# Kernel tuning notes

Hardware: AMD Instinct MI355X
Metric: run time of the kernel (lower is better)

The kernel has to match this reference:

```python
import jax, jax.numpy as jnp
import numpy as np

B, T, C, H = 8, 1024, 1024, 16
NEG = -1000000000.0
EPS = 1e-12


def setup_inputs() -> dict:
    key = jax.random.key(0)
    ks = jax.random.split(key, 12)
    s = 0.02  # keep pre-softmax logits in a sane range
    return {
        "x": jax.random.normal(ks[0], (B, T, C), jnp.float32),
        "mask": jax.random.randint(ks[1], (B, T), 0, 2, jnp.int32),
        "Wq": jax.random.normal(ks[2], (C, C), jnp.float32) * s,
        "bq": jax.random.normal(ks[3], (C,), jnp.float32) * s,
        "Wk": jax.random.normal(ks[4], (C, C), jnp.float32) * s,
        "bk": jax.random.normal(ks[5], (C,), jnp.float32) * s,
        "Wv": jax.random.normal(ks[6], (C, C), jnp.float32) * s,
        "bv": jax.random.normal(ks[7], (C,), jnp.float32) * s,
        "Wp": jax.random.normal(ks[8], (C, C), jnp.float32) * s,
        "bp": jax.random.normal(ks[9], (C,), jnp.float32) * s,
        "ln_w": jnp.ones((C,), jnp.float32),
        "ln_b": jnp.zeros((C,), jnp.float32),
    }


def reference(x, mask, Wq, bq, Wk, bk, Wv, bv, Wp, bp, ln_w, ln_b):
    Bx, Tx, Cx = x.shape
    hd = Cx // H
    # torch nn.Linear: y = x @ W.T + b
    def lin(inp, W, b):
        return inp @ W.T + b

    def split_heads(t):  # [B,T,C] -> [B,H,T,hd]
        return t.reshape(Bx, Tx, H, hd).transpose(0, 2, 1, 3)

    q = split_heads(lin(x, Wq, bq))
    k = split_heads(lin(x, Wk, bk))
    v = split_heads(lin(x, Wv, bv))

    att = jnp.einsum("bhqd,bhkd->bhqk", q, k) * (1.0 / jnp.sqrt(jnp.float32(hd)))
    # mask [B,T] masks key positions; broadcast to [B,1,1,T]
    att = jnp.where(mask[:, None, None, :] == 0, NEG, att)
    # stable softmax (manual max-subtract, matching original)
    att = jax.nn.softmax(att, axis=-1)
    # dropout prob 0.0 -> identity (eval-mode faithful)
    y = jnp.einsum("bhqk,bhkd->bhqd", att, v)
    y = y.transpose(0, 2, 1, 3).reshape(Bx, Tx, Cx)
    y = lin(y, Wp, bp)
    # residual + LayerNorm(eps=1e-12)
    z = y + x
    mu = jnp.mean(z, axis=-1, keepdims=True)
    var = jnp.mean(jnp.square(z - mu), axis=-1, keepdims=True)
    out = (z - mu) * jax.lax.rsqrt(var + EPS) * ln_w + ln_b
    return out
```

## Files before the change

kernel.cpp:

```cpp
#include <hip/hip_runtime.h>
#include <stdint.h>

#define B_ 8
#define T_ 1024
#define C_ 1024
#define H_ 16
#define HD 64
#define M_TOT (B_ * T_)

using f32x4 = __attribute__((ext_vector_type(4))) float;
using s16x8 = __attribute__((ext_vector_type(8))) short;
using i32x4 = __attribute__((ext_vector_type(4))) int;

__device__ __forceinline__ unsigned short f2bf(float f) {
  unsigned int u = __builtin_bit_cast(unsigned int, f);
  unsigned int r = (u + 0x7fffu + ((u >> 16) & 1u)) >> 16;
  return (unsigned short)r;
}
__device__ __forceinline__ float bf2f(unsigned short s) {
  unsigned int u = ((unsigned int)s) << 16;
  return __builtin_bit_cast(float, u);
}

__device__ __forceinline__ void gload_lds16(const void* g, void* l) {
  __builtin_amdgcn_global_load_lds(
      (const __attribute__((address_space(1))) unsigned int*)g,
      (__attribute__((address_space(3))) unsigned int*)l, 16, 0, 0);
}

__global__ __launch_bounds__(256) void k_convert(
    const float* __restrict__ x, const float* __restrict__ wq,
    const float* __restrict__ wk, const float* __restrict__ wv,
    const float* __restrict__ wp, const float* __restrict__ bq,
    const float* __restrict__ bk, const float* __restrict__ bv,
    const int* __restrict__ maskp, unsigned short* __restrict__ xb,
    unsigned short* __restrict__ wqkv, unsigned short* __restrict__ wpb,
    float* __restrict__ bias_cat, unsigned int* __restrict__ mpair) {
  const long n_x = (long)M_TOT * C_;
  const long W_ELT = (long)C_ * C_;
  const long total4 = (n_x + 4 * W_ELT) >> 2;
  for (long i4 = (long)blockIdx.x * blockDim.x + threadIdx.x; i4 < total4;
       i4 += (long)gridDim.x * blockDim.x) {
    long i = i4 << 2;
    const float* src;
    unsigned short* dst;
    if (i < n_x) {
      src = x + i;
      dst = xb + i;
    } else {
      long off = i - n_x;
      int which = (int)(off >> 20);
      long wo = off & (W_ELT - 1);
      if (which < 3) {
        src = (which == 0 ? wq : which == 1 ? wk : wv) + wo;
        dst = wqkv + which * W_ELT + wo;
      } else {
        src = wp + wo;
        dst = wpb + wo;
      }
    }
    float4 v = *(const float4*)src;
    ushort4 u;
    u.x = f2bf(v.x); u.y = f2bf(v.y); u.z = f2bf(v.z); u.w = f2bf(v.w);
    *(ushort4*)dst = u;
  }
  int t = blockIdx.x * blockDim.x + threadIdx.x;
  if (t < 3 * C_) {
    float v = t < C_ ? bq[t] : (t < 2 * C_ ? bk[t - C_] : bv[t - 2 * C_]);
    bias_cat[t] = v;
  }
  if (t < B_ * T_ / 2) {
    const int* mr = maskp + t * 2;
    mpair[t] = (mr[0] ? 0xFFFFu : 0u) | (mr[1] ? 0xFFFF0000u : 0u);
  }
}

template <int EPI>
__global__ __launch_bounds__(256, 2) void k_gemm(
    const unsigned short* __restrict__ A, const unsigned short* __restrict__ Bm,
    const float* __restrict__ bias, unsigned short* __restrict__ q_ws,
    unsigned short* __restrict__ k_ws, unsigned short* __restrict__ vt_ws,
    const unsigned short* __restrict__ xres16, unsigned short* __restrict__ z16) {
  __shared__ unsigned short Al[2][128 * 64];
  __shared__ unsigned short Bl[2][128 * 64];
  const int tid = threadIdx.x, lane = tid & 63, w = tid >> 6;
  const int lc = lane & 15, lr = lane >> 4;
  const int wm = w >> 1, wn = w & 1;
  const int GX = (EPI == 0) ? 24 : 8;
  const int NWG = GX * 64;
  int flat = blockIdx.y * GX + blockIdx.x;
  int swz = (flat & 7) * (NWG / 8) + (flat >> 3);
  const int m0 = (swz / GX) * 128, n0 = (swz % GX) * 128;
  const char* Ab = (const char*)A;
  const char* Bb = (const char*)Bm;

  f32x4 acc[4][4] = {};

  auto stage = [&](int buf, int kt) {
#pragma unroll
    for (int i = 0; i < 4; ++i) {
      int g = i * 256 + tid;
      int row = g >> 3, gr = g & 7;
      gload_lds16(Ab + (long)(m0 + row) * 2048 + kt * 128 + ((gr ^ (row & 7)) << 4),
                  (char*)Al[buf] + (i * 256 + w * 64) * 16);
    }
#pragma unroll
    for (int i = 0; i < 4; ++i) {
      int g = i * 256 + tid;
      int row = g >> 3, gr = g & 7;
      gload_lds16(Bb + (long)(n0 + row) * 2048 + kt * 128 + ((gr ^ (row & 7)) << 4),
                  (char*)Bl[buf] + (i * 256 + w * 64) * 16);
    }
  };

  stage(0, 0);
  stage(1, 1);
  asm volatile("s_waitcnt vmcnt(8)" ::: "memory");
  __builtin_amdgcn_sched_barrier(0);
  __builtin_amdgcn_s_barrier();
  __builtin_amdgcn_sched_barrier(0);

#pragma unroll
  for (int kt = 0; kt < 16; ++kt) {
    const int cur = kt & 1;
    const char* Ac = (const char*)Al[cur];
    const char* Bc = (const char*)Bl[cur];
    s16x8 af0[4], bf0[4];
#pragma unroll
    for (int mf = 0; mf < 4; ++mf) {
      int ar = wm * 64 + mf * 16 + lc;
      af0[mf] = *(const s16x8*)(Ac + ar * 128 + ((lr ^ (ar & 7)) << 4));
    }
#pragma unroll
    for (int nf = 0; nf < 4; ++nf) {
      int br = wn * 64 + nf * 16 + lc;
      bf0[nf] = *(const s16x8*)(Bc + br * 128 + ((lr ^ (br & 7)) << 4));
    }
#pragma unroll
    for (int mf = 0; mf < 4; ++mf)
#pragma unroll
      for (int nf = 0; nf < 4; ++nf)
        acc[mf][nf] = __builtin_amdgcn_mfma_f32_16x16x32_bf16(af0[mf], bf0[nf],
                                                              acc[mf][nf], 0, 0, 0);
    s16x8 af1[4], bf1[4];
#pragma unroll
    for (int mf = 0; mf < 4; ++mf) {
      int ar = wm * 64 + mf * 16 + lc;
      af1[mf] = *(const s16x8*)(Ac + ar * 128 + (((4 + lr) ^ (ar & 7)) << 4));
    }
#pragma unroll
    for (int nf = 0; nf < 4; ++nf) {
      int br = wn * 64 + nf * 16 + lc;
      bf1[nf] = *(const s16x8*)(Bc + br * 128 + (((4 + lr) ^ (br & 7)) << 4));
    }
    asm volatile("s_waitcnt lgkmcnt(0)" ::: "memory");
    __builtin_amdgcn_sched_barrier(0);
    __builtin_amdgcn_s_barrier();
    __builtin_amdgcn_sched_barrier(0);
    if (kt + 2 < 16) stage(cur, kt + 2);
    __builtin_amdgcn_s_setprio(1);
#pragma unroll
    for (int mf = 0; mf < 4; ++mf)
#pragma unroll
      for (int nf = 0; nf < 4; ++nf)
        acc[mf][nf] = __builtin_amdgcn_mfma_f32_16x16x32_bf16(af1[mf], bf1[nf],
                                                              acc[mf][nf], 0, 0, 0);
    __builtin_amdgcn_s_setprio(0);
    if (kt + 2 < 16)
      asm volatile("s_waitcnt vmcnt(8)" ::: "memory");
    else
      asm volatile("s_waitcnt vmcnt(0)" ::: "memory");
    __builtin_amdgcn_sched_barrier(0);
    __builtin_amdgcn_s_barrier();
    __builtin_amdgcn_sched_barrier(0);
  }

  if (EPI == 0) {
#pragma unroll
    for (int mf = 0; mf < 4; ++mf)
#pragma unroll
      for (int nf = 0; nf < 4; ++nf) {
        int gn = n0 + wn * 64 + nf * 16 + lc;
        int which = gn >> 10, nn = gn & 1023;
        int hh = nn >> 6, dd = nn & 63;
        float bia = bias[gn];
        if (which == 2) {
          int gm = m0 + wm * 64 + mf * 16 + lr * 4;
          int bb = gm >> 10, tt = gm & 1023;
          ushort4 pk;
          pk.x = f2bf(acc[mf][nf][0] + bia);
          pk.y = f2bf(acc[mf][nf][1] + bia);
          pk.z = f2bf(acc[mf][nf][2] + bia);
          pk.w = f2bf(acc[mf][nf][3] + bia);
          *(ushort4*)&vt_ws[((long)(bb * H_ + hh) * HD + dd) * T_ + tt] = pk;
        } else {
          unsigned short* dst = (which == 0) ? q_ws : k_ws;
          float scl = (which == 0) ? 0.18033688011112042f : 1.0f;
#pragma unroll
          for (int i = 0; i < 4; ++i) {
            int gm = m0 + wm * 64 + mf * 16 + lr * 4 + i;
            int bb = gm >> 10, tt = gm & 1023;
            dst[((long)(bb * H_ + hh) * T_ + tt) * HD + dd] =
                f2bf((acc[mf][nf][i] + bia) * scl);
          }
        }
      }
  } else {
#pragma unroll
    for (int mf = 0; mf < 4; ++mf)
#pragma unroll
      for (int nf = 0; nf < 4; ++nf) {
        int gn = n0 + wn * 64 + nf * 16 + lc;
        float bia = bias[gn];
#pragma unroll
        for (int i = 0; i < 4; ++i) {
          int gm = m0 + wm * 64 + mf * 16 + lr * 4 + i;
          long idx = (long)gm * C_ + gn;
          z16[idx] = f2bf(acc[mf][nf][i] + bia + bf2f(xres16[idx]));
        }
      }
  }
}

__global__ __launch_bounds__(256, 2) void k_attn(
    const unsigned short* __restrict__ Qp, const unsigned short* __restrict__ Kp,
    const unsigned short* __restrict__ Vtp, const unsigned int* __restrict__ mpairp,
    unsigned short* __restrict__ Yp) {
  __shared__ unsigned short Kl[2][64 * 64];
  __shared__ unsigned short Vl[2][64 * 64];
  const int tid = threadIdx.x, lane = tid & 63, w = tid >> 6;
  const int bid = blockIdx.x;
  const int xcd = bid & 7, slot = bid >> 3;
  const int bh = xcd * 16 + (slot >> 2);
  const int qt = slot & 3;
  const int b = bh >> 4, h = bh & 15;
  const int lc = lane & 15, lr = lane >> 4;
  const int q0 = qt * 256 + w * 64;

  const unsigned short* qbase = Qp + ((long)bh * T_ + q0) * HD;
  s16x8 aq[4][2];
#pragma unroll
  for (int g = 0; g < 4; ++g) {
    aq[g][0] = *(const s16x8*)(qbase + (g * 16 + lc) * HD + lr * 8);
    aq[g][1] = *(const s16x8*)(qbase + (g * 16 + lc) * HD + 32 + lr * 8);
  }

  s16x8 ones;
#pragma unroll
  for (int j = 0; j < 8; ++j) ones[j] = (short)0x3F80;

  f32x4 o[4][4] = {};
  f32x4 ol[4] = {};

  const char* kb_g = (const char*)(Kp + (long)bh * T_ * HD);
  const char* vb_g = (const char*)(Vtp + (long)bh * HD * T_);
  const unsigned int* mrow2 = mpairp + b * (T_ / 2);

  auto stage = [&](int buf, int kt) {
#pragma unroll
    for (int it = 0; it < 2; ++it) {
      int f = it * 4096 + w * 1024 + lane * 16;
      int row = f >> 7;
      int swz = (f & 127) ^ ((row & 7) << 4);
      gload_lds16(kb_g + (long)kt * 8192 + (f & ~127) + swz,
                  (char*)Kl[buf] + it * 4096 + w * 1024);
      gload_lds16(vb_g + (long)row * (T_ * 2) + kt * 128 + swz,
                  (char*)Vl[buf] + it * 4096 + w * 1024);
    }
  };

  stage(0, 0);
  __syncthreads();

  const int s01 = lc + ((lane & 16) << 1);
  const int s23 = s01 + 16;
  const bool hi = (lane >= 32);

  int cur = 0;
  for (int kt = 0; kt < T_ / 64; ++kt) {
    if (kt + 1 < T_ / 64) stage(cur ^ 1, kt + 1);

    f32x4 s[4][4];
    const char* kl = (const char*)Kl[cur];
#pragma unroll
    for (int kf = 0; kf < 4; ++kf) {
      int key = kf * 16 + lc;
      s16x8 kb0 = *(const s16x8*)(kl + ((key * 128 + lr * 16) ^ ((key & 7) << 4)));
      s16x8 kb1 = *(const s16x8*)(kl + ((key * 128 + 64 + lr * 16) ^ ((key & 7) << 4)));
#pragma unroll
      for (int g = 0; g < 4; ++g) {
        f32x4 z = {};
        z = __builtin_amdgcn_mfma_f32_16x16x32_bf16(kb0, aq[g][0], z, 0, 0, 0);
        z = __builtin_amdgcn_mfma_f32_16x16x32_bf16(kb1, aq[g][1], z, 0, 0, 0);
        s[g][kf] = z;
      }
    }

    unsigned int mw[4][2];
#pragma unroll
    for (int kf = 0; kf < 4; ++kf) {
      mw[kf][0] = mrow2[kt * 32 + kf * 8 + lr * 2];
      mw[kf][1] = mrow2[kt * 32 + kf * 8 + lr * 2 + 1];
    }

    unsigned int pk[4][4][2];
#pragma unroll
    for (int g = 0; g < 4; ++g)
#pragma unroll
      for (int kf = 0; kf < 4; ++kf) {
        unsigned int u0 = __builtin_bit_cast(unsigned int, __builtin_amdgcn_exp2f(s[g][kf][0]));
        unsigned int u1 = __builtin_bit_cast(unsigned int, __builtin_amdgcn_exp2f(s[g][kf][1]));
        unsigned int u2 = __builtin_bit_cast(unsigned int, __builtin_amdgcn_exp2f(s[g][kf][2]));
        unsigned int u3 = __builtin_bit_cast(unsigned int, __builtin_amdgcn_exp2f(s[g][kf][3]));
        pk[g][kf][0] = ((u1 & 0xFFFF0000u) | (u0 >> 16)) & mw[kf][0];
        pk[g][kf][1] = ((u3 & 0xFFFF0000u) | (u2 >> 16)) & mw[kf][1];
      }

#pragma unroll
    for (int kc = 0; kc < 2; ++kc) {
      s16x8 ap[4];
#pragma unroll
      for (int g = 0; g < 4; ++g) {
        unsigned int A0 = pk[g][kc * 2][0], A1 = pk[g][kc * 2][1];
        unsigned int B0 = pk[g][kc * 2 + 1][0], B1 = pk[g][kc * 2 + 1][1];
        unsigned int w0a = __shfl((int)A0, s01, 64), w0b = __shfl((int)B0, s01, 64);
        unsigned int w1a = __shfl((int)A1, s01, 64), w1b = __shfl((int)B1, s01, 64);
        unsigned int w2a = __shfl((int)A0, s23, 64), w2b = __shfl((int)B0, s23, 64);
        unsigned int w3a = __shfl((int)A1, s23, 64), w3b = __shfl((int)B1, s23, 64);
        i32x4 wv;
        wv[0] = (int)(hi ? w0b : w0a);
        wv[1] = (int)(hi ? w1b : w1a);
        wv[2] = (int)(hi ? w2b : w2a);
        wv[3] = (int)(hi ? w3b : w3a);
        ap[g] = __builtin_bit_cast(s16x8, wv);
      }
      int koff = kc * 64 + lr * 16;
      __builtin_amdgcn_s_setprio(1);
#pragma unroll
      for (int g = 0; g < 4; ++g)
        ol[g] = __builtin_amdgcn_mfma_f32_16x16x32_bf16(ones, ap[g], ol[g], 0, 0, 0);
#pragma unroll
      for (int nf = 0; nf < 4; ++nf) {
        int drow = nf * 16 + lc;
        s16x8 vb = *(const s16x8*)((const char*)Vl[cur] +
                                   ((drow * 128 + koff) ^ ((drow & 7) << 4)));
#pragma unroll
        for (int g = 0; g < 4; ++g)
          o[g][nf] = __builtin_amdgcn_mfma_f32_16x16x32_bf16(vb, ap[g], o[g][nf], 0, 0, 0);
      }
      __builtin_amdgcn_s_setprio(0);
    }
    __syncthreads();
    cur ^= 1;
  }

#pragma unroll
  for (int g = 0; g < 4; ++g) {
    float rl = 1.0f / ol[g][0];
    unsigned short* yrow = Yp + ((long)(b * T_ + q0 + g * 16 + lc)) * C_ + h * 64;
#pragma unroll
    for (int nf = 0; nf < 4; ++nf) {
      ushort4 pw;
      pw.x = f2bf(o[g][nf][0] * rl);
      pw.y = f2bf(o[g][nf][1] * rl);
      pw.z = f2bf(o[g][nf][2] * rl);
      pw.w = f2bf(o[g][nf][3] * rl);
      *(ushort4*)(yrow + nf * 16 + lr * 4) = pw;
    }
  }
}

__global__ __launch_bounds__(256) void k_ln(const unsigned short* __restrict__ z16,
                                            const float* __restrict__ lw,
                                            const float* __restrict__ lb,
                                            float* __restrict__ out) {
  const int row = blockIdx.x;
  ushort4 v16 = ((const ushort4*)(z16 + (long)row * C_))[threadIdx.x];
  float4 v;
  v.x = bf2f(v16.x); v.y = bf2f(v16.y); v.z = bf2f(v16.z); v.w = bf2f(v16.w);
  float s = v.x + v.y + v.z + v.w;
  float s2 = v.x * v.x + v.y * v.y + v.z * v.z + v.w * v.w;
#pragma unroll
  for (int d = 1; d < 64; d <<= 1) {
    s += __shfl_xor(s, d, 64);
    s2 += __shfl_xor(s2, d, 64);
  }
  __shared__ float rs[4], rq[4];
  int wv_ = threadIdx.x >> 6;
  if ((threadIdx.x & 63) == 0) { rs[wv_] = s; rq[wv_] = s2; }
  __syncthreads();
  s = rs[0] + rs[1] + rs[2] + rs[3];
  s2 = rq[0] + rq[1] + rq[2] + rq[3];
  float mu = s * (1.0f / C_);
  float var = s2 * (1.0f / C_) - mu * mu;
  float inv = rsqrtf(var + 1e-12f);
  float4 wv4 = ((const float4*)lw)[threadIdx.x];
  float4 bv4 = ((const float4*)lb)[threadIdx.x];
  float4 ov;
  ov.x = (v.x - mu) * inv * wv4.x + bv4.x;
  ov.y = (v.y - mu) * inv * wv4.y + bv4.y;
  ov.z = (v.z - mu) * inv * wv4.z + bv4.z;
  ov.w = (v.w - mu) * inv * wv4.w + bv4.w;
  ((float4*)(out + (long)row * C_))[threadIdx.x] = ov;
}

extern "C" void kernel_launch(void* const* d_in, const int* in_sizes, int n_in,
                              void* d_out, int out_size, void* d_ws,
                              size_t ws_size, hipStream_t stream) {
  const float* x = (const float*)d_in[0];
  const int* mask = (const int*)d_in[1];
  const float* Wq = (const float*)d_in[2];
  const float* bq = (const float*)d_in[3];
  const float* Wk = (const float*)d_in[4];
  const float* bk = (const float*)d_in[5];
  const float* Wv = (const float*)d_in[6];
  const float* bv = (const float*)d_in[7];
  const float* Wp = (const float*)d_in[8];
  const float* bp = (const float*)d_in[9];
  const float* lnw = (const float*)d_in[10];
  const float* lnb = (const float*)d_in[11];
  float* out = (float*)d_out;

  char* ws = (char*)d_ws;
  const size_t MB = 1024 * 1024;
  unsigned short* xb = (unsigned short*)(ws);
  unsigned short* q_ws = (unsigned short*)(ws + 16 * MB);
  unsigned short* k_ws = (unsigned short*)(ws + 32 * MB);
  unsigned short* vt_ws = (unsigned short*)(ws + 48 * MB);
  unsigned short* y_ws = (unsigned short*)(ws + 64 * MB);
  unsigned short* wqkv = (unsigned short*)(ws + 80 * MB);
  unsigned short* wpb = (unsigned short*)(ws + 86 * MB);
  float* bias_cat = (float*)(ws + 88 * MB);
  unsigned int* mpair = (unsigned int*)(ws + 88 * MB + 16384);
  unsigned short* z16 = (unsigned short*)(ws + 48 * MB);

  k_convert<<<dim3(2048), dim3(256), 0, stream>>>(x, Wq, Wk, Wv, Wp, bq, bk, bv,
                                                  mask, xb, wqkv, wpb, bias_cat,
                                                  mpair);
  k_gemm<0><<<dim3(24, 64), dim3(256), 0, stream>>>(
      xb, wqkv, bias_cat, q_ws, k_ws, vt_ws, nullptr, nullptr);
  k_attn<<<dim3(512), dim3(256), 0, stream>>>(q_ws, k_ws, vt_ws, mpair, y_ws);
  k_gemm<1><<<dim3(8, 64), dim3(256), 0, stream>>>(
      y_ws, wpb, bp, nullptr, nullptr, nullptr, xb, z16);
  k_ln<<<dim3(8192), dim3(256), 0, stream>>>(z16, lnw, lnb, out);
}
```

Measured before the change: 163.9 us.

## Use 256x256 tiles with 8 waves and interleaved staging for QKV GEMM

Splits the QKV projection into its own kernel with 256x256 output tiles, 512 threads (8 waves in a 2x4 layout), and a 384-block grid. Global-to-LDS loads for the next k-step are split into four quarter stages and interleaved with four MFMA sub-phases, each wave holding 8x4 accumulators. The larger tile raises arithmetic intensity and reuse of the staged A and B tiles. In exchange it uses 128 KB of LDS per block, more registers, and fewer blocks, so wave-level parallelism and occupancy drop.

```diff
diff --git a/kernel.cpp b/kernel.cpp
--- a/kernel.cpp
+++ b/kernel.cpp
@@ -75,18 +75,193 @@
   }
 }
 
-template <int EPI>
-__global__ __launch_bounds__(256, 2) void k_gemm(
+__global__ __launch_bounds__(512, 2) void k_gemm_qkv(
     const unsigned short* __restrict__ A, const unsigned short* __restrict__ Bm,
     const float* __restrict__ bias, unsigned short* __restrict__ q_ws,
-    unsigned short* __restrict__ k_ws, unsigned short* __restrict__ vt_ws,
-    const unsigned short* __restrict__ xres16, unsigned short* __restrict__ z16) {
+    unsigned short* __restrict__ k_ws, unsigned short* __restrict__ vt_ws) {
+  __shared__ unsigned short Al[2][256 * 64];
+  __shared__ unsigned short Bl[2][256 * 64];
+  const int tid = threadIdx.x, lane = tid & 63, w = tid >> 6;
+  const int lc = lane & 15, lr = lane >> 4;
+  const int wm = w >> 2, wn = w & 3;
+  const int GX = 12;
+  const int NWG = GX * 32;
+  int flat = blockIdx.y * GX + blockIdx.x;
+  int swz = (flat & 7) * (NWG / 8) + (flat >> 3);
+  const int m0 = (swz / GX) * 256, n0 = (swz % GX) * 256;
+  const char* Ab = (const char*)A;
+  const char* Bb = (const char*)Bm;
+
+  f32x4 acc[8][4] = {};
+
+  auto stageA = [&](int buf, int kt, int half) {
+#pragma unroll
+    for (int j = 0; j < 2; ++j) {
+      int i = half * 2 + j;
+      int g = i * 512 + tid;
+      int row = g >> 3, gr = g & 7;
+      gload_lds16(Ab + (long)(m0 + row) * 2048 + kt * 128 + ((gr ^ (row & 7)) << 4),
+                  (char*)Al[buf] + (long)(i * 512 + w * 64) * 16);
+    }
+  };
+  auto stageB = [&](int buf, int kt, int half) {
+#pragma unroll
+    for (int j = 0; j < 2; ++j) {
+      int i = half * 2 + j;
+      int g = i * 512 + tid;
+      int row = g >> 3, gr = g & 7;
+      gload_lds16(Bb + (long)(n0 + row) * 2048 + kt * 128 + ((gr ^ (row & 7)) << 4),
+                  (char*)Bl[buf] + (long)(i * 512 + w * 64) * 16);
+    }
+  };
+
+  stageA(0, 0, 0);
+  stageB(0, 0, 0);
+  stageA(0, 0, 1);
+  stageB(0, 0, 1);
+
+#pragma unroll
+  for (int kt = 0; kt < 16; ++kt) {
+    const int cur = kt & 1, nxt = cur ^ 1;
+    const bool have = (kt + 1 < 16);
+    const char* Ac = (const char*)Al[cur];
+    const char* Bc = (const char*)Bl[cur];
+    s16x8 aLo[4][2], aHi[4][2], bfr[4][2];
+
+    if (have) stageA(nxt, kt + 1, 0);
+    if (have)
+      asm volatile("s_waitcnt vmcnt(2)" ::: "memory");
+    else
+      asm volatile("s_waitcnt vmcnt(0)" ::: "memory");
+    __builtin_amdgcn_sched_barrier(0);
+    __builtin_amdgcn_s_barrier();
+    __builtin_amdgcn_sched_barrier(0);
+#pragma unroll
+    for (int mf = 0; mf < 4; ++mf) {
+      int ar = wm * 128 + mf * 16 + lc;
+#pragma unroll
+      for (int kk = 0; kk < 2; ++kk)
+        aLo[mf][kk] = *(const s16x8*)(Ac + ar * 128 + (((kk * 4 + lr) ^ (ar & 7)) << 4));
+    }
+#pragma unroll
+    for (int nf = 0; nf < 2; ++nf) {
+      int br = wn * 64 + nf * 16 + lc;
+#pragma unroll
+      for (int kk = 0; kk < 2; ++kk)
+        bfr[nf][kk] = *(const s16x8*)(Bc + br * 128 + (((kk * 4 + lr) ^ (br & 7)) << 4));
+    }
+    asm volatile("s_waitcnt lgkmcnt(0)" ::: "memory");
+    __builtin_amdgcn_sched_barrier(0);
+    __builtin_amdgcn_s_setprio(1);
+#pragma unroll
+    for (int mf = 0; mf < 4; ++mf)
+#pragma unroll
+      for (int nf = 0; nf < 2; ++nf)
+#pragma unroll
+        for (int kk = 0; kk < 2; ++kk)
+          acc[mf][nf] = __builtin_amdgcn_mfma_f32_16x16x32_bf16(
+              aLo[mf][kk], bfr[nf][kk], acc[mf][nf], 0, 0, 0);
+    __builtin_amdgcn_s_setprio(0);
+
+    if (have) stageB(nxt, kt + 1, 0);
+#pragma unroll
+    for (int nf = 2; nf < 4; ++nf) {
+      int br = wn * 64 + nf * 16 + lc;
+#pragma unroll
+      for (int kk = 0; kk < 2; ++kk)
+        bfr[nf][kk] = *(const s16x8*)(Bc + br * 128 + (((kk * 4 + lr) ^ (br & 7)) << 4));
+    }
+    asm volatile("s_waitcnt lgkmcnt(0)" ::: "memory");
+    __builtin_amdgcn_sched_barrier(0);
+    __builtin_amdgcn_s_setprio(1);
+#pragma unroll
+    for (int mf = 0; mf < 4; ++mf)
+#pragma unroll
+      for (int nf = 2; nf < 4; ++nf)
+#pragma unroll
+        for (int kk = 0; kk < 2; ++kk)
+          acc[mf][nf] = __builtin_amdgcn_mfma_f32_16x16x32_bf16(
+              aLo[mf][kk], bfr[nf][kk], acc[mf][nf], 0, 0, 0);
+    __builtin_amdgcn_s_setprio(0);
+
+    if (have) stageA(nxt, kt + 1, 1);
+#pragma unroll
+    for (int mf = 0; mf < 4; ++mf) {
+      int ar = wm * 128 + 64 + mf * 16 + lc;
+#pragma unroll
+      for (int kk = 0; kk < 2; ++kk)
+        aHi[mf][kk] = *(const s16x8*)(Ac + ar * 128 + (((kk * 4 + lr) ^ (ar & 7)) << 4));
+    }
+    asm volatile("s_waitcnt lgkmcnt(0)" ::: "memory");
+    __builtin_amdgcn_sched_barrier(0);
+    __builtin_amdgcn_s_setprio(1);
+#pragma unroll
+    for (int mf = 0; mf < 4; ++mf)
+#pragma unroll
+      for (int nf = 2; nf < 4; ++nf)
+#pragma unroll
+        for (int kk = 0; kk < 2; ++kk)
+          acc[4 + mf][nf] = __builtin_amdgcn_mfma_f32_16x16x32_bf16(
+              aHi[mf][kk], bfr[nf][kk], acc[4 + mf][nf], 0, 0, 0);
+    __builtin_amdgcn_s_setprio(0);
+
+    if (have) stageB(nxt, kt + 1, 1);
+    __builtin_amdgcn_s_setprio(1);
+#pragma unroll
+    for (int mf = 0; mf < 4; ++mf)
+#pragma unroll
+      for (int nf = 0; nf < 2; ++nf)
+#pragma unroll
+        for (int kk = 0; kk < 2; ++kk)
+          acc[4 + mf][nf] = __builtin_amdgcn_mfma_f32_16x16x32_bf16(
+              aHi[mf][kk], bfr[nf][kk], acc[4 + mf][nf], 0, 0, 0);
+    __builtin_amdgcn_s_setprio(0);
+    __builtin_amdgcn_sched_barrier(0);
+    __builtin_amdgcn_s_barrier();
+    __builtin_amdgcn_sched_barrier(0);
+  }
+
+#pragma unroll
+  for (int mf = 0; mf < 8; ++mf)
+#pragma unroll
+    for (int nf = 0; nf < 4; ++nf) {
+      int gn = n0 + wn * 64 + nf * 16 + lc;
+      int which = gn >> 10, nn = gn & 1023;
+      int hh = nn >> 6, dd = nn & 63;
+      float bia = bias[gn];
+      if (which == 2) {
+        int gm = m0 + wm * 128 + mf * 16 + lr * 4;
+        int bb = gm >> 10, tt = gm & 1023;
+        ushort4 pk;
+        pk.x = f2bf(acc[mf][nf][0] + bia);
+        pk.y = f2bf(acc[mf][nf][1] + bia);
+        pk.z = f2bf(acc[mf][nf][2] + bia);
+        pk.w = f2bf(acc[mf][nf][3] + bia);
+        *(ushort4*)&vt_ws[((long)(bb * H_ + hh) * HD + dd) * T_ + tt] = pk;
+      } else {
+        unsigned short* dst = (which == 0) ? q_ws : k_ws;
+        float scl = (which == 0) ? 0.18033688011112042f : 1.0f;
+#pragma unroll
+        for (int i = 0; i < 4; ++i) {
+          int gm = m0 + wm * 128 + mf * 16 + lr * 4 + i;
+          int bb = gm >> 10, tt = gm & 1023;
+          dst[((long)(bb * H_ + hh) * T_ + tt) * HD + dd] =
+              f2bf((acc[mf][nf][i] + bia) * scl);
+        }
+      }
+    }
+}
+
+__global__ __launch_bounds__(256, 2) void k_gemm_proj(
+    const unsigned short* __restrict__ A, const unsigned short* __restrict__ Bm,
+    const float* __restrict__ bias, const unsigned short* __restrict__ xres16,
+    unsigned short* __restrict__ z16) {
   __shared__ unsigned short Al[2][128 * 64];
   __shared__ unsigned short Bl[2][128 * 64];
   const int tid = threadIdx.x, lane = tid & 63, w = tid >> 6;
   const int lc = lane & 15, lr = lane >> 4;
   const int wm = w >> 1, wn = w & 1;
-  const int GX = (EPI == 0) ? 24 : 8;
+  const int GX = 8;
   const int NWG = GX * 64;
   int flat = blockIdx.y * GX + blockIdx.x;
   int swz = (flat & 7) * (NWG / 8) + (flat >> 3);
@@ -175,51 +350,19 @@
     __builtin_amdgcn_sched_barrier(0);
   }
 
-  if (EPI == 0) {
-#pragma unroll
-    for (int mf = 0; mf < 4; ++mf)
-#pragma unroll
-      for (int nf = 0; nf < 4; ++nf) {
-        int gn = n0 + wn * 64 + nf * 16 + lc;
-        int which = gn >> 10, nn = gn & 1023;
-        int hh = nn >> 6, dd = nn & 63;
-        float bia = bias[gn];
-        if (which == 2) {
-          int gm = m0 + wm * 64 + mf * 16 + lr * 4;
-          int bb = gm >> 10, tt = gm & 1023;
-          ushort4 pk;
-          pk.x = f2bf(acc[mf][nf][0] + bia);
-          pk.y = f2bf(acc[mf][nf][1] + bia);
-          pk.z = f2bf(acc[mf][nf][2] + bia);
-          pk.w = f2bf(acc[mf][nf][3] + bia);
-          *(ushort4*)&vt_ws[((long)(bb * H_ + hh) * HD + dd) * T_ + tt] = pk;
-        } else {
-          unsigned short* dst = (which == 0) ? q_ws : k_ws;
-          float scl = (which == 0) ? 0.18033688011112042f : 1.0f;
-#pragma unroll
-          for (int i = 0; i < 4; ++i) {
-            int gm = m0 + wm * 64 + mf * 16 + lr * 4 + i;
-            int bb = gm >> 10, tt = gm & 1023;
-            dst[((long)(bb * H_ + hh) * T_ + tt) * HD + dd] =
-                f2bf((acc[mf][nf][i] + bia) * scl);
-          }
-        }
-      }
-  } else {
-#pragma unroll
-    for (int mf = 0; mf < 4; ++mf)
-#pragma unroll
-      for (int nf = 0; nf < 4; ++nf) {
-        int gn = n0 + wn * 64 + nf * 16 + lc;
-        float bia = bias[gn];
-#pragma unroll
-        for (int i = 0; i < 4; ++i) {
-          int gm = m0 + wm * 64 + mf * 16 + lr * 4 + i;
-          long idx = (long)gm * C_ + gn;
-          z16[idx] = f2bf(acc[mf][nf][i] + bia + bf2f(xres16[idx]));
-        }
-      }
-  }
+#pragma unroll
+  for (int mf = 0; mf < 4; ++mf)
+#pragma unroll
+    for (int nf = 0; nf < 4; ++nf) {
+      int gn = n0 + wn * 64 + nf * 16 + lc;
+      float bia = bias[gn];
+#pragma unroll
+      for (int i = 0; i < 4; ++i) {
+        int gm = m0 + wm * 64 + mf * 16 + lr * 4 + i;
+        long idx = (long)gm * C_ + gn;
+        z16[idx] = f2bf(acc[mf][nf][i] + bia + bf2f(xres16[idx]));
+      }
+    }
 }
 
 __global__ __launch_bounds__(256, 2) void k_attn(
@@ -437,10 +580,9 @@
   k_convert<<<dim3(2048), dim3(256), 0, stream>>>(x, Wq, Wk, Wv, Wp, bq, bk, bv,
                                                   mask, xb, wqkv, wpb, bias_cat,
                                                   mpair);
-  k_gemm<0><<<dim3(24, 64), dim3(256), 0, stream>>>(
-      xb, wqkv, bias_cat, q_ws, k_ws, vt_ws, nullptr, nullptr);
+  k_gemm_qkv<<<dim3(12, 32), dim3(512), 0, stream>>>(xb, wqkv, bias_cat, q_ws,
+                                                     k_ws, vt_ws);
   k_attn<<<dim3(512), dim3(256), 0, stream>>>(q_ws, k_ws, vt_ws, mpair, y_ws);
-  k_gemm<1><<<dim3(8, 64), dim3(256), 0, stream>>>(
-      y_ws, wpb, bp, nullptr, nullptr, nullptr, xb, z16);
+  k_gemm_proj<<<dim3(8, 64), dim3(256), 0, stream>>>(y_ws, wpb, bp, xb, z16);
   k_ln<<<dim3(8192), dim3(256), 0, stream>>>(z16, lnw, lnb, out);
 }
```

Measured after the change: 174.5 us. +6.4%, slower.
